# Kernel optimization log

Hardware: AMD Instinct MI355X
Metric: run time of the kernel (lower is better)

Reference implementation:

```python
import jax, jax.numpy as jnp
import numpy as np


def _conv1x1(x, W, b):
    # 1x1 conv == per-pixel linear: x [B,H,W,Cin] @ W [Cin,Cout] + b
    return jnp.einsum('bhwc,cd->bhwd', x, W) + b


def setup_inputs() -> dict:
    key = jax.random.key(0)
    ks = jax.random.split(key, 5)
    B, H, W, C = 4, 64, 64, 256
    Ck = C // 8
    x = jax.random.normal(ks[0], (B, H, W, C), dtype=jnp.float32)
    Wf = jax.random.normal(ks[1], (C, Ck), dtype=jnp.float32) * 0.05
    Wg = jax.random.normal(ks[2], (C, Ck), dtype=jnp.float32) * 0.05
    Wh = jax.random.normal(ks[3], (C, C), dtype=jnp.float32) * 0.05
    Wv = jax.random.normal(ks[4], (C, C), dtype=jnp.float32) * 0.05
    return {
        'x': x,
        'Wf': Wf, 'bf': jnp.zeros((Ck,), jnp.float32),
        'Wg': Wg, 'bg': jnp.zeros((Ck,), jnp.float32),
        'Wh': Wh, 'bh': jnp.zeros((C,), jnp.float32),
        'Wv': Wv, 'bv': jnp.zeros((C,), jnp.float32),
    }


def reference(x, Wf, bf, Wg, bg, Wh, bh, Wv, bv):
    B, H, W, C = x.shape
    f = _conv1x1(x, Wf, bf).reshape(B, H * W, -1)   # [B,N,C/8]
    g = _conv1x1(x, Wg, bg).reshape(B, H * W, -1)   # [B,N,C/8]
    hm = _conv1x1(x, Wh, bh).reshape(B, H * W, C)   # [B,N,C]
    # unscaled attention: s = g @ f^T, softmax over last axis
    s = jnp.einsum('bnk,bmk->bnm', g, f)            # [B,N,N]
    beta = jax.nn.softmax(s, axis=-1)
    o = jnp.einsum('bnm,bmc->bnc', beta, hm)        # [B,N,C]
    o = o.reshape(B, H, W, C)
    o = _conv1x1(o, Wv, bv)
    return x + o
```

## Files before the change

kernel.cpp:

```cpp
#include <hip/hip_runtime.h>
#include <math.h>


typedef unsigned short u16;
typedef __attribute__((ext_vector_type(8))) short  bf16x8;
typedef __attribute__((ext_vector_type(4))) float  f32x4;

__device__ inline u16 f2bf(float x) {
    unsigned u = __float_as_uint(x);
    unsigned r = (u + 0x7fffu + ((u >> 16) & 1u)) >> 16;
    return (u16)r;
}

__device__ inline float bf2f(short s) {
    return __uint_as_float(((unsigned)(u16)s) << 16);
}

__device__ inline bf16x8 cvt8(float4 a, float4 b) {
    bf16x8 r;
    r[0] = (short)f2bf(a.x); r[1] = (short)f2bf(a.y);
    r[2] = (short)f2bf(a.z); r[3] = (short)f2bf(a.w);
    r[4] = (short)f2bf(b.x); r[5] = (short)f2bf(b.y);
    r[6] = (short)f2bf(b.z); r[7] = (short)f2bf(b.w);
    return r;
}

#define ASYNC_CP16(gp, lp)                                                     \
    __builtin_amdgcn_global_load_lds(                                          \
        (const __attribute__((address_space(1))) void*)(gp),                   \
        (__attribute__((address_space(3))) void*)(lp), 16, 0, 0)

#define LOG2E 1.4426950408889634f

__device__ inline size_t vfrag_off(int b, int cg, int kc, int quad, int l16) {
    return ((((size_t)b * 16 + cg) * 128 + kc) << 9) + (quad << 7) + (l16 << 3);
}

__global__ __launch_bounds__(256) void prep_w(
    const float* __restrict__ Wf, const float* __restrict__ Wg,
    const float* __restrict__ Wh, const float* __restrict__ Wv,
    u16* __restrict__ wT)
{
    const int n = blockIdx.x;
    const int k = threadIdx.x;
    float v;
    if (n < 32)        v = Wf[(size_t)k * 32 + n];
    else if (n < 64)   v = Wg[(size_t)k * 32 + n - 32] * LOG2E;
    else if (n < 320)  v = Wh[(size_t)k * 256 + n - 64];
    else               v = Wv[(size_t)k * 256 + n - 320];
    wT[(size_t)n * 256 + k] = f2bf(v);
}

__global__ __launch_bounds__(256) void proj_mfma2(
    const float* __restrict__ x, const u16* __restrict__ wT,
    const float* __restrict__ bfv, const float* __restrict__ bgv,
    const float* __restrict__ bhv,
    u16* __restrict__ fg, u16* __restrict__ hmt)
{
    __shared__ float xl[16 * 268];

    const int t    = threadIdx.x;
    const int w    = t >> 6;
    const int lane = t & 63;
    const int quad = lane >> 4;
    const int l16  = lane & 15;
    const int m0   = blockIdx.x * 16;
    const int wb   = w * 80;

#pragma unroll
    for (int i = 0; i < 4; ++i) {
        int idx = i * 256 + t;
        int row = idx >> 6;
        int c4  = (idx & 63) << 2;
        float4 v = *reinterpret_cast<const float4*>(
            x + (size_t)(m0 + row) * 256 + c4);
        *reinterpret_cast<float4*>(&xl[row * 268 + c4]) = v;
    }
    __syncthreads();

    f32x4 acc[5];
#pragma unroll
    for (int nt = 0; nt < 5; ++nt)
#pragma unroll
        for (int r = 0; r < 4; ++r) acc[nt][r] = 0.f;

#pragma unroll 2
    for (int ks = 0; ks < 8; ++ks) {
        const float* xp = &xl[l16 * 268 + ks * 32 + quad * 8];
        float4 a0 = *reinterpret_cast<const float4*>(xp);
        float4 a1 = *reinterpret_cast<const float4*>(xp + 4);
        bf16x8 afrag = cvt8(a0, a1);
#pragma unroll
        for (int nt = 0; nt < 5; ++nt) {
            bf16x8 bfrag = *reinterpret_cast<const bf16x8*>(
                wT + (size_t)(wb + nt * 16 + l16) * 256 + ks * 32 + quad * 8);
            acc[nt] = __builtin_amdgcn_mfma_f32_16x16x32_bf16(
                afrag, bfrag, acc[nt], 0, 0, 0);
        }
    }

    const int bb   = m0 >> 12;
    const int npix = m0 & 4095;
#pragma unroll
    for (int nt = 0; nt < 5; ++nt) {
        int col = wb + nt * 16 + l16;
        if (col < 64) {
            float bias = (col < 32) ? bfv[col] : bgv[col - 32] * LOG2E;
            int row = m0 + quad * 4;
#pragma unroll
            for (int r = 0; r < 4; ++r)
                fg[(size_t)(row + r) * 64 + col] = f2bf(acc[nt][r] + bias);
        } else {
            int c = col - 64;
            float bias = bhv[c];
            int n0 = npix + quad * 4;
            ushort4 hv;
            hv.x = f2bf(acc[nt][0] + bias);
            hv.y = f2bf(acc[nt][1] + bias);
            hv.z = f2bf(acc[nt][2] + bias);
            hv.w = f2bf(acc[nt][3] + bias);
            size_t off = ((((size_t)bb * 16 + (c >> 4)) * 128 + (n0 >> 5))
                          << 9) + (((n0 >> 3) & 3) << 7) + ((c & 15) << 3) +
                         (n0 & 7);
            *reinterpret_cast<ushort4*>(hmt + off) = hv;
        }
    }
}

__global__ __launch_bounds__(256) void attn5(
    const u16* __restrict__ fg, const u16* __restrict__ hmt,
    u16* __restrict__ obf, float* __restrict__ lpart, int ksl)
{
    __shared__ u16 fl[2][4096];
    __shared__ u16 pl[8192];
    __shared__ float lfin[64];

    const int t    = threadIdx.x;
    const int w    = t >> 6;
    const int lane = t & 63;
    const int quad = lane >> 4;
    const int l16  = lane & 15;

    int b, qt, ks;
    if (ksl == 1) {
        const int u   = blockIdx.x;
        const int xcd = u & 7;
        b = xcd >> 1;
        const int v = ((u >> 3) << 1) | (xcd & 1);
        qt = v >> 1;
        ks = v & 1;
    } else {
        ks = 0;
        qt = blockIdx.x & 63;
        b  = blockIdx.x >> 6;
    }
    const int nkt = 32 >> ksl;
    const int kt0 = ks * nkt;

    const size_t fg_base = (size_t)b * 4096 * 64;

    const bf16x8 gfrag = *reinterpret_cast<const bf16x8*>(
        fg + fg_base + (size_t)(qt * 64 + w * 16 + l16) * 64 + 32 + quad * 8);

    f32x4 oacc[4][4];
#pragma unroll
    for (int mt = 0; mt < 4; ++mt)
#pragma unroll
        for (int nt = 0; nt < 4; ++nt)
#pragma unroll
            for (int r = 0; r < 4; ++r) oacc[mt][nt][r] = 0.f;

    float lsum[4] = {0.f, 0.f, 0.f, 0.f};
    const f32x4 zero4 = {0.f, 0.f, 0.f, 0.f};

    {
        const u16* gp = fg + fg_base +
            (size_t)(kt0 * 128 + (2 * w) * 16 + l16) * 64 + quad * 8;
        ASYNC_CP16(gp, &fl[0][(2 * w) * 512]);
        ASYNC_CP16(gp + 16 * 64, &fl[0][(2 * w + 1) * 512]);
    }

    for (int it = 0; it < nkt; ++it) {
        const int kt  = kt0 + it;
        const int buf = it & 1;
        __syncthreads();

        bf16x8 vbr[4][4];
#pragma unroll
        for (int nt = 0; nt < 4; ++nt)
#pragma unroll
            for (int kh = 0; kh < 4; ++kh)
                vbr[nt][kh] = *reinterpret_cast<const bf16x8*>(
                    hmt + vfrag_off(b, w * 4 + nt, kt * 4 + kh, quad, l16));

        if (it + 1 < nkt) {
            const u16* gp = fg + fg_base +
                (size_t)((kt + 1) * 128 + (2 * w) * 16 + l16) * 64 + quad * 8;
            ASYNC_CP16(gp, &fl[buf ^ 1][(2 * w) * 512]);
            ASYNC_CP16(gp + 16 * 64, &fl[buf ^ 1][(2 * w + 1) * 512]);
        }

        f32x4 sacc[8];
#pragma unroll
        for (int ct = 0; ct < 8; ++ct) {
            bf16x8 fb = *reinterpret_cast<const bf16x8*>(
                &fl[buf][ct * 512 + quad * 128 + l16 * 8]);
            sacc[ct] = __builtin_amdgcn_mfma_f32_16x16x32_bf16(
                gfrag, fb, zero4, 0, 0, 0);
        }

#pragma unroll
        for (int ct = 0; ct < 8; ++ct) {
#pragma unroll
            for (int r = 0; r < 4; ++r) {
                float p = __builtin_amdgcn_exp2f(sacc[ct][r]);
                lsum[r] += p;
                int row = w * 16 + quad * 4 + r;
                int key = ct * 16 + l16;
                pl[(key >> 3) * 512 + row * 8 + (key & 7)] = f2bf(p);
            }
        }
        __syncthreads();

#pragma unroll
        for (int kh = 0; kh < 4; ++kh) {
            bf16x8 pa[4];
#pragma unroll
            for (int mt = 0; mt < 4; ++mt)
                pa[mt] = *reinterpret_cast<const bf16x8*>(
                    &pl[(kh * 4 + quad) * 512 + (mt * 16 + l16) * 8]);
#pragma unroll
            for (int nt = 0; nt < 4; ++nt)
#pragma unroll
                for (int mt = 0; mt < 4; ++mt)
                    oacc[mt][nt] = __builtin_amdgcn_mfma_f32_16x16x32_bf16(
                        pa[mt], vbr[nt][kh], oacc[mt][nt], 0, 0, 0);
        }
    }

#pragma unroll
    for (int r = 0; r < 4; ++r) {
        float s = lsum[r];
        s += __shfl_xor(s, 1);
        s += __shfl_xor(s, 2);
        s += __shfl_xor(s, 4);
        s += __shfl_xor(s, 8);
        lsum[r] = s;
    }
    if (l16 == 0) {
#pragma unroll
        for (int r = 0; r < 4; ++r) {
            lfin[w * 16 + quad * 4 + r] = lsum[r];
            lpart[((size_t)ks << 14) + b * 4096 + qt * 64 + w * 16 +
                  quad * 4 + r] = lsum[r];
        }
    }
    __syncthreads();

#pragma unroll
    for (int mt = 0; mt < 4; ++mt) {
        f32x4 lv = *reinterpret_cast<const f32x4*>(&lfin[mt * 16 + quad * 4]);
        float inv[4];
#pragma unroll
        for (int r = 0; r < 4; ++r) inv[r] = 1.f / lv[r];
        const int row16 = b * 256 + qt * 4 + mt;
#pragma unroll
        for (int nt = 0; nt < 4; ++nt) {
            int ksc = w * 2 + (nt >> 1);
            int qc  = (nt & 1) * 2 + (l16 >> 3);
            u16* op = obf + ((size_t)ks << 22) +
                (((size_t)row16 * 8 + ksc) << 9) + (qc << 7) + (l16 & 7);
#pragma unroll
            for (int r = 0; r < 4; ++r)
                op[(quad * 4 + r) * 8] = f2bf(oacc[mt][nt][r] * inv[r]);
        }
    }
}

__global__ __launch_bounds__(256, 2) void attn8(
    const u16* __restrict__ fg, const u16* __restrict__ hmt,
    u16* __restrict__ obf, float* __restrict__ lpart, int ksl)
{
    __shared__ u16 fl[2][4096];
    __shared__ u16 pl[16 * 1024];
    __shared__ float lfin[128];

    const int t    = threadIdx.x;
    const int w    = t >> 6;
    const int lane = t & 63;
    const int quad = lane >> 4;
    const int l16  = lane & 15;

    const int u   = blockIdx.x;
    const int xcd = u & 7;
    const int b   = xcd >> 1;
    const int v   = ((u >> 3) << 1) | (xcd & 1);
    const int qt  = v >> ksl;
    const int ks  = v & ((1 << ksl) - 1);

    const int nkt = 32 >> ksl;
    const int kt0 = ks * nkt;

    const size_t fg_base = (size_t)b * 4096 * 64;

    bf16x8 gfrag[2];
#pragma unroll
    for (int h2 = 0; h2 < 2; ++h2)
        gfrag[h2] = *reinterpret_cast<const bf16x8*>(
            fg + fg_base +
            (size_t)(qt * 128 + w * 32 + h2 * 16 + l16) * 64 + 32 + quad * 8);

    f32x4 oacc[8][4];
#pragma unroll
    for (int mt = 0; mt < 8; ++mt)
#pragma unroll
        for (int nt = 0; nt < 4; ++nt)
#pragma unroll
            for (int r = 0; r < 4; ++r) oacc[mt][nt][r] = 0.f;

    float lsum[2][4] = {{0.f, 0.f, 0.f, 0.f}, {0.f, 0.f, 0.f, 0.f}};
    const f32x4 zero4 = {0.f, 0.f, 0.f, 0.f};

    {
        const u16* gp = fg + fg_base +
            (size_t)(kt0 * 128 + (2 * w) * 16 + l16) * 64 + quad * 8;
        ASYNC_CP16(gp, &fl[0][(2 * w) * 512]);
        ASYNC_CP16(gp + 16 * 64, &fl[0][(2 * w + 1) * 512]);
    }

    for (int it = 0; it < nkt; ++it) {
        const int kt  = kt0 + it;
        const int buf = it & 1;
        __syncthreads();

        if (it + 1 < nkt) {
            const u16* gp = fg + fg_base +
                (size_t)((kt + 1) * 128 + (2 * w) * 16 + l16) * 64 + quad * 8;
            ASYNC_CP16(gp, &fl[buf ^ 1][(2 * w) * 512]);
            ASYNC_CP16(gp + 16 * 64, &fl[buf ^ 1][(2 * w + 1) * 512]);
        }

        {
            f32x4 sacc[8];
#pragma unroll
            for (int ct = 0; ct < 8; ++ct) {
                bf16x8 fb = *reinterpret_cast<const bf16x8*>(
                    &fl[buf][ct * 512 + quad * 128 + l16 * 8]);
                sacc[ct] = __builtin_amdgcn_mfma_f32_16x16x32_bf16(
                    gfrag[0], fb, zero4, 0, 0, 0);
            }
#pragma unroll
            for (int ct = 0; ct < 8; ++ct) {
#pragma unroll
                for (int r = 0; r < 4; ++r) {
                    float p = __builtin_amdgcn_exp2f(sacc[ct][r]);
                    lsum[0][r] += p;
                    int row = w * 32 + quad * 4 + r;
                    int key = ct * 16 + l16;
                    pl[(key >> 3) * 1024 + row * 8 + (key & 7)] = f2bf(p);
                }
            }
        }

        bf16x8 va[4][2];
#pragma unroll
        for (int nt = 0; nt < 4; ++nt)
#pragma unroll
            for (int j = 0; j < 2; ++j)
                va[nt][j] = *reinterpret_cast<const bf16x8*>(
                    hmt + vfrag_off(b, w * 4 + nt, kt * 4 + j, quad, l16));

        {
            f32x4 sacc[8];
#pragma unroll
            for (int ct = 0; ct < 8; ++ct) {
                bf16x8 fb = *reinterpret_cast<const bf16x8*>(
                    &fl[buf][ct * 512 + quad * 128 + l16 * 8]);
                sacc[ct] = __builtin_amdgcn_mfma_f32_16x16x32_bf16(
                    gfrag[1], fb, zero4, 0, 0, 0);
            }
#pragma unroll
            for (int ct = 0; ct < 8; ++ct) {
#pragma unroll
                for (int r = 0; r < 4; ++r) {
                    float p = __builtin_amdgcn_exp2f(sacc[ct][r]);
                    lsum[1][r] += p;
                    int row = w * 32 + 16 + quad * 4 + r;
                    int key = ct * 16 + l16;
                    pl[(key >> 3) * 1024 + row * 8 + (key & 7)] = f2bf(p);
                }
            }
        }
        __syncthreads();

#pragma unroll
        for (int kh = 0; kh < 2; ++kh) {
#pragma unroll
            for (int mh = 0; mh < 2; ++mh) {
                bf16x8 pa[4];
#pragma unroll
                for (int m = 0; m < 4; ++m)
                    pa[m] = *reinterpret_cast<const bf16x8*>(
                        &pl[(kh * 4 + quad) * 1024 +
                            ((mh * 4 + m) * 16 + l16) * 8]);
#pragma unroll
                for (int nt = 0; nt < 4; ++nt)
#pragma unroll
                    for (int m = 0; m < 4; ++m)
                        oacc[mh * 4 + m][nt] =
                            __builtin_amdgcn_mfma_f32_16x16x32_bf16(
                                pa[m], va[nt][kh], oacc[mh * 4 + m][nt],
                                0, 0, 0);
            }
        }

        bf16x8 vb[4][2];
#pragma unroll
        for (int nt = 0; nt < 4; ++nt)
#pragma unroll
            for (int j = 0; j < 2; ++j)
                vb[nt][j] = *reinterpret_cast<const bf16x8*>(
                    hmt + vfrag_off(b, w * 4 + nt, kt * 4 + 2 + j, quad, l16));
#pragma unroll
        for (int kh = 2; kh < 4; ++kh) {
#pragma unroll
            for (int mh = 0; mh < 2; ++mh) {
                bf16x8 pa[4];
#pragma unroll
                for (int m = 0; m < 4; ++m)
                    pa[m] = *reinterpret_cast<const bf16x8*>(
                        &pl[(kh * 4 + quad) * 1024 +
                            ((mh * 4 + m) * 16 + l16) * 8]);
#pragma unroll
                for (int nt = 0; nt < 4; ++nt)
#pragma unroll
                    for (int m = 0; m < 4; ++m)
                        oacc[mh * 4 + m][nt] =
                            __builtin_amdgcn_mfma_f32_16x16x32_bf16(
                                pa[m], vb[nt][kh - 2], oacc[mh * 4 + m][nt],
                                0, 0, 0);
            }
        }
    }

#pragma unroll
    for (int h2 = 0; h2 < 2; ++h2) {
#pragma unroll
        for (int r = 0; r < 4; ++r) {
            float s = lsum[h2][r];
            s += __shfl_xor(s, 1);
            s += __shfl_xor(s, 2);
            s += __shfl_xor(s, 4);
            s += __shfl_xor(s, 8);
            lsum[h2][r] = s;
        }
    }
    if (l16 == 0) {
#pragma unroll
        for (int h2 = 0; h2 < 2; ++h2)
#pragma unroll
            for (int r = 0; r < 4; ++r) {
                int row = w * 32 + h2 * 16 + quad * 4 + r;
                lfin[row] = lsum[h2][r];
                lpart[((size_t)ks << 14) + b * 4096 + qt * 128 + row] =
                    lsum[h2][r];
            }
    }
    __syncthreads();

#pragma unroll
    for (int mt = 0; mt < 8; ++mt) {
        f32x4 lv = *reinterpret_cast<const f32x4*>(&lfin[mt * 16 + quad * 4]);
        float inv[4];
#pragma unroll
        for (int r = 0; r < 4; ++r) inv[r] = 1.f / lv[r];
        const int row16 = b * 256 + qt * 8 + mt;
#pragma unroll
        for (int nt = 0; nt < 4; ++nt) {
            int ksc = w * 2 + (nt >> 1);
            int qc  = (nt & 1) * 2 + (l16 >> 3);
            u16* op = obf + ((size_t)ks << 22) +
                (((size_t)row16 * 8 + ksc) << 9) + (qc << 7) + (l16 & 7);
#pragma unroll
            for (int r = 0; r < 4; ++r)
                op[(quad * 4 + r) * 8] = f2bf(oacc[mt][nt][r] * inv[r]);
        }
    }
}

__global__ __launch_bounds__(256) void final_mfma5(
    const u16* __restrict__ obf, const float* __restrict__ lpart, int S,
    const u16* __restrict__ wT, const float* __restrict__ bvv,
    const float* __restrict__ x, float* __restrict__ out)
{
    __shared__ u16 ol[16384];

    const int t    = threadIdx.x;
    const int w    = t >> 6;
    const int lane = t & 63;
    const int quad = lane >> 4;
    const int l16  = lane & 15;
    const int m0   = blockIdx.x * 16;
    const int wb   = w * 64;

    const int ni = S * 2;
    for (int i = 0; i < ni; ++i) {
        int gi = w * ni + i;
        int s  = gi >> 3;
        int ks = gi & 7;
        const u16* gp = obf + ((size_t)s << 22) +
            (((size_t)(m0 >> 4) * 8 + ks) << 9) + lane * 8;
        ASYNC_CP16(gp, &ol[gi * 512]);
    }

    float wgt[4];
    {
        int row = m0 + l16;
        float lv[4];
        float tot = 0.f;
#pragma unroll
        for (int s = 0; s < 4; ++s) {
            lv[s] = (s < S) ? lpart[((size_t)s << 14) + row] : 0.f;
            tot += lv[s];
        }
        float inv = 1.f / tot;
#pragma unroll
        for (int s = 0; s < 4; ++s) wgt[s] = lv[s] * inv;
    }
    __syncthreads();

    f32x4 acc[4];
#pragma unroll
    for (int nt = 0; nt < 4; ++nt)
#pragma unroll
        for (int r = 0; r < 4; ++r) acc[nt][r] = 0.f;

#pragma unroll 2
    for (int ks = 0; ks < 8; ++ks) {
        bf16x8 afrag;
        {
            bf16x8 v0 = *reinterpret_cast<const bf16x8*>(
                &ol[ks * 512 + (quad * 16 + l16) * 8]);
            if (S == 1) {
                afrag = v0;
            } else {
                float tacc[8];
#pragma unroll
                for (int j = 0; j < 8; ++j) tacc[j] = wgt[0] * bf2f(v0[j]);
#pragma unroll
                for (int s = 1; s < 4; ++s) {
                    if (s < S) {
                        bf16x8 vs = *reinterpret_cast<const bf16x8*>(
                            &ol[(s * 8 + ks) * 512 + (quad * 16 + l16) * 8]);
#pragma unroll
                        for (int j = 0; j < 8; ++j)
                            tacc[j] = fmaf(wgt[s], bf2f(vs[j]), tacc[j]);
                    }
                }
#pragma unroll
                for (int j = 0; j < 8; ++j) afrag[j] = (short)f2bf(tacc[j]);
            }
        }
#pragma unroll
        for (int nt = 0; nt < 4; ++nt) {
            bf16x8 bfrag = *reinterpret_cast<const bf16x8*>(
                wT + (size_t)(320 + wb + nt * 16 + l16) * 256 +
                ks * 32 + quad * 8);
            acc[nt] = __builtin_amdgcn_mfma_f32_16x16x32_bf16(
                afrag, bfrag, acc[nt], 0, 0, 0);
        }
    }

#pragma unroll
    for (int nt = 0; nt < 4; ++nt) {
        int col = wb + nt * 16 + l16;
        float bias = bvv[col];
        int row = m0 + quad * 4;
#pragma unroll
        for (int r = 0; r < 4; ++r) {
            size_t off = (size_t)(row + r) * 256 + col;
            out[off] = acc[nt][r] + bias + x[off];
        }
    }
}

extern "C" void kernel_launch(void* const* d_in, const int* in_sizes, int n_in,
                              void* d_out, int out_size, void* d_ws, size_t ws_size,
                              hipStream_t stream)
{
    const float* x  = (const float*)d_in[0];
    const float* Wf = (const float*)d_in[1];
    const float* bf = (const float*)d_in[2];
    const float* Wg = (const float*)d_in[3];
    const float* bg = (const float*)d_in[4];
    const float* Wh = (const float*)d_in[5];
    const float* bh = (const float*)d_in[6];
    const float* Wv = (const float*)d_in[7];
    const float* bv = (const float*)d_in[8];
    float* out = (float*)d_out;

    const int M = 16384;

    const size_t base_b = (size_t)M * 64 * 2 + (size_t)4 * 256 * 4096 * 2 +
                          (size_t)576 * 256 * 2;
    const size_t per_s  = (size_t)M * 4 + (size_t)M * 256 * 2;
    int ksl = 0;
    if (ws_size >= base_b + 4 * per_s)      ksl = 2;
    else if (ws_size >= base_b + 2 * per_s) ksl = 1;
    const int S = 1 << ksl;

    u16*   fgbuf = (u16*)d_ws;
    u16*   hmt   = fgbuf + (size_t)M * 64;
    u16*   wT    = hmt + (size_t)4 * 256 * 4096;
    float* lpart = (float*)(wT + (size_t)576 * 256);
    u16*   obf   = (u16*)(lpart + (size_t)S * M);

    dim3 blk(256);

    prep_w<<<dim3(576), blk, 0, stream>>>(Wf, Wg, Wh, Wv, wT);
    proj_mfma2<<<dim3(M / 16), blk, 0, stream>>>(x, wT, bf, bg, bh, fgbuf, hmt);
    if (ksl == 2)
        attn8<<<dim3(512), blk, 0, stream>>>(fgbuf, hmt, obf, lpart, ksl);
    else
        attn5<<<dim3(256 * S), blk, 0, stream>>>(fgbuf, hmt, obf, lpart, ksl);
    final_mfma5<<<dim3(M / 16), blk, 0, stream>>>(
        obf, lpart, S, wT, bv, x, out);
}
```

Measured before the change: 170.5 us.

## Defer softmax normalization into final projection and accumulate split partials via MFMA

The attention kernels now store unnormalized partial outputs and skip the shared-memory row-sum exchange, a __syncthreads and the per-element divide. The final kernel no longer blends the split-K partials with per-split weights and a bf16 repack. Instead it feeds every partial straight into the MFMA chain, since the Wv projection is linear, and scales by the inverse of the total row sum in the epilogue. This trades CUDA-core blend work for S times more MFMAs in the final kernel. It also stores unnormalized values in bf16, which stays correct only because all splits share a common softmax reference.

```diff
diff --git a/kernel.cpp b/kernel.cpp
--- a/kernel.cpp
+++ b/kernel.cpp
@@ -133,7 +133,6 @@
 {
     __shared__ u16 fl[2][4096];
     __shared__ u16 pl[8192];
-    __shared__ float lfin[64];
 
     const int t    = threadIdx.x;
     const int w    = t >> 6;
@@ -249,20 +248,13 @@
     }
     if (l16 == 0) {
 #pragma unroll
-        for (int r = 0; r < 4; ++r) {
-            lfin[w * 16 + quad * 4 + r] = lsum[r];
+        for (int r = 0; r < 4; ++r)
             lpart[((size_t)ks << 14) + b * 4096 + qt * 64 + w * 16 +
                   quad * 4 + r] = lsum[r];
-        }
-    }
-    __syncthreads();
+    }
 
 #pragma unroll
     for (int mt = 0; mt < 4; ++mt) {
-        f32x4 lv = *reinterpret_cast<const f32x4*>(&lfin[mt * 16 + quad * 4]);
-        float inv[4];
-#pragma unroll
-        for (int r = 0; r < 4; ++r) inv[r] = 1.f / lv[r];
         const int row16 = b * 256 + qt * 4 + mt;
 #pragma unroll
         for (int nt = 0; nt < 4; ++nt) {
@@ -272,7 +264,7 @@
                 (((size_t)row16 * 8 + ksc) << 9) + (qc << 7) + (l16 & 7);
 #pragma unroll
             for (int r = 0; r < 4; ++r)
-                op[(quad * 4 + r) * 8] = f2bf(oacc[mt][nt][r] * inv[r]);
+                op[(quad * 4 + r) * 8] = f2bf(oacc[mt][nt][r]);
         }
     }
 }
@@ -283,7 +275,6 @@
 {
     __shared__ u16 fl[2][4096];
     __shared__ u16 pl[16 * 1024];
-    __shared__ float lfin[128];
 
     const int t    = threadIdx.x;
     const int w    = t >> 6;
@@ -461,19 +452,13 @@
 #pragma unroll
             for (int r = 0; r < 4; ++r) {
                 int row = w * 32 + h2 * 16 + quad * 4 + r;
-                lfin[row] = lsum[h2][r];
                 lpart[((size_t)ks << 14) + b * 4096 + qt * 128 + row] =
                     lsum[h2][r];
             }
     }
-    __syncthreads();
 
 #pragma unroll
     for (int mt = 0; mt < 8; ++mt) {
-        f32x4 lv = *reinterpret_cast<const f32x4*>(&lfin[mt * 16 + quad * 4]);
-        float inv[4];
-#pragma unroll
-        for (int r = 0; r < 4; ++r) inv[r] = 1.f / lv[r];
         const int row16 = b * 256 + qt * 8 + mt;
 #pragma unroll
         for (int nt = 0; nt < 4; ++nt) {
@@ -483,17 +468,18 @@
                 (((size_t)row16 * 8 + ksc) << 9) + (qc << 7) + (l16 & 7);
 #pragma unroll
             for (int r = 0; r < 4; ++r)
-                op[(quad * 4 + r) * 8] = f2bf(oacc[mt][nt][r] * inv[r]);
-        }
-    }
-}
-
-__global__ __launch_bounds__(256) void final_mfma5(
+                op[(quad * 4 + r) * 8] = f2bf(oacc[mt][nt][r]);
+        }
+    }
+}
+
+__global__ __launch_bounds__(256) void final_mfma7(
     const u16* __restrict__ obf, const float* __restrict__ lpart, int S,
     const u16* __restrict__ wT, const float* __restrict__ bvv,
     const float* __restrict__ x, float* __restrict__ out)
 {
     __shared__ u16 ol[16384];
+    __shared__ float linv[16];
 
     const int t    = threadIdx.x;
     const int w    = t >> 6;
@@ -513,19 +499,12 @@
         ASYNC_CP16(gp, &ol[gi * 512]);
     }
 
-    float wgt[4];
-    {
-        int row = m0 + l16;
-        float lv[4];
+    if (t < 16) {
         float tot = 0.f;
 #pragma unroll
-        for (int s = 0; s < 4; ++s) {
-            lv[s] = (s < S) ? lpart[((size_t)s << 14) + row] : 0.f;
-            tot += lv[s];
-        }
-        float inv = 1.f / tot;
-#pragma unroll
-        for (int s = 0; s < 4; ++s) wgt[s] = lv[s] * inv;
+        for (int s = 0; s < 4; ++s)
+            if (s < S) tot += lpart[((size_t)s << 14) + m0 + t];
+        linv[t] = 1.f / tot;
     }
     __syncthreads();
 
@@ -535,39 +514,24 @@
 #pragma unroll
         for (int r = 0; r < 4; ++r) acc[nt][r] = 0.f;
 
-#pragma unroll 2
+#pragma unroll
     for (int ks = 0; ks < 8; ++ks) {
-        bf16x8 afrag;
-        {
-            bf16x8 v0 = *reinterpret_cast<const bf16x8*>(
-                &ol[ks * 512 + (quad * 16 + l16) * 8]);
-            if (S == 1) {
-                afrag = v0;
-            } else {
-                float tacc[8];
-#pragma unroll
-                for (int j = 0; j < 8; ++j) tacc[j] = wgt[0] * bf2f(v0[j]);
-#pragma unroll
-                for (int s = 1; s < 4; ++s) {
-                    if (s < S) {
-                        bf16x8 vs = *reinterpret_cast<const bf16x8*>(
-                            &ol[(s * 8 + ks) * 512 + (quad * 16 + l16) * 8]);
-#pragma unroll
-                        for (int j = 0; j < 8; ++j)
-                            tacc[j] = fmaf(wgt[s], bf2f(vs[j]), tacc[j]);
-                    }
-                }
-#pragma unroll
-                for (int j = 0; j < 8; ++j) afrag[j] = (short)f2bf(tacc[j]);
-            }
-        }
-#pragma unroll
-        for (int nt = 0; nt < 4; ++nt) {
-            bf16x8 bfrag = *reinterpret_cast<const bf16x8*>(
+        bf16x8 bfrag[4];
+#pragma unroll
+        for (int nt = 0; nt < 4; ++nt)
+            bfrag[nt] = *reinterpret_cast<const bf16x8*>(
                 wT + (size_t)(320 + wb + nt * 16 + l16) * 256 +
                 ks * 32 + quad * 8);
-            acc[nt] = __builtin_amdgcn_mfma_f32_16x16x32_bf16(
-                afrag, bfrag, acc[nt], 0, 0, 0);
+#pragma unroll
+        for (int s = 0; s < 4; ++s) {
+            if (s < S) {
+                bf16x8 afrag = *reinterpret_cast<const bf16x8*>(
+                    &ol[(s * 8 + ks) * 512 + lane * 8]);
+#pragma unroll
+                for (int nt = 0; nt < 4; ++nt)
+                    acc[nt] = __builtin_amdgcn_mfma_f32_16x16x32_bf16(
+                        afrag, bfrag[nt], acc[nt], 0, 0, 0);
+            }
         }
     }
 
@@ -579,7 +543,7 @@
 #pragma unroll
         for (int r = 0; r < 4; ++r) {
             size_t off = (size_t)(row + r) * 256 + col;
-            out[off] = acc[nt][r] + bias + x[off];
+            out[off] = acc[nt][r] * linv[quad * 4 + r] + bias + x[off];
         }
     }
 }
@@ -623,6 +587,6 @@
         attn8<<<dim3(512), blk, 0, stream>>>(fgbuf, hmt, obf, lpart, ksl);
     else
         attn5<<<dim3(256 * S), blk, 0, stream>>>(fgbuf, hmt, obf, lpart, ksl);
-    final_mfma5<<<dim3(M / 16), blk, 0, stream>>>(
+    final_mfma7<<<dim3(M / 16), blk, 0, stream>>>(
         obf, lpart, S, wT, bv, x, out);
 }
```

After: 173.5 us. About the same (+1.7%).
